# Kernel optimization log

Hardware: AMD Instinct MI355X
Metric: run time of the kernel (lower is better)

The kernel has to match this reference:

```python
import jax, jax.numpy as jnp
import numpy as np

HIDDEN_DIM = 1024
NUM_HEADS = 16
HEAD_DIM = HIDDEN_DIM // NUM_HEADS


def setup_inputs() -> dict:
    key = jax.random.key(0)
    k1, k2, k3 = jax.random.split(key, 3)
    B, S, D = 2, 2048, HIDDEN_DIM
    x = jax.random.normal(k1, (B, S, D), dtype=jnp.float32)
    attention_mask = jnp.ones((B, S), dtype=jnp.int32)
    scale = 1.0 / np.sqrt(D)
    W_qkv = jax.random.normal(k2, (D, 3 * D), dtype=jnp.float32) * scale
    b_qkv = jnp.zeros((3 * D,), dtype=jnp.float32)
    W_out = jax.random.normal(k3, (D, D), dtype=jnp.float32) * scale
    b_out = jnp.zeros((D,), dtype=jnp.float32)
    return {"x": x, "attention_mask": attention_mask,
            "W_qkv": W_qkv, "b_qkv": b_qkv, "W_out": W_out, "b_out": b_out}


def reference(x, attention_mask, W_qkv, b_qkv, W_out, b_out):
    B, S, D = x.shape
    H, hd = NUM_HEADS, HEAD_DIM
    qkv = x @ W_qkv + b_qkv                     # [B,S,3D]
    # Faithful to torch: view to [B,S,H,3*hd] THEN chunk last dim (per-head interleaving)
    qkv = qkv.reshape(B, S, H, 3 * hd)
    q, k, v = jnp.split(qkv, 3, axis=-1)        # each [B,S,H,hd]
    scores = jnp.einsum('bqhd,bkhd->bhqk', q, k) / np.sqrt(hd)  # [B,H,S,S]
    mask = attention_mask[:, None, None, :]     # broadcast over heads, queries
    scores = jnp.where(mask == 0, -jnp.inf, scores)
    weights = jax.nn.softmax(scores, axis=-1)
    out = jnp.einsum('bhqk,bkhd->bqhd', weights, v).reshape(B, S, D)
    return out @ W_out + b_out
```

## Files before the change

kernel.cpp:

```cpp
#include <hip/hip_runtime.h>

#define SDIM 2048
#define NHEADS 16
#define HD 64

typedef __attribute__((ext_vector_type(8))) short bf16x8;
typedef __attribute__((ext_vector_type(8))) unsigned short u16x8;
typedef __attribute__((ext_vector_type(4))) float f32x4;
typedef unsigned short u16;

static __device__ __forceinline__ u16 f2bf(float f) {
  unsigned u = __builtin_bit_cast(unsigned, f);
  u += 0x7fffu + ((u >> 16) & 1u);
  return (u16)(u >> 16);
}

static __device__ __forceinline__ unsigned cvt_pk_bf16(float lo, float hi) {
  unsigned r;
  asm("v_cvt_pk_bf16_f32 %0, %1, %2" : "=v"(r) : "v"(lo), "v"(hi));
  return r;
}

static __device__ __forceinline__ f32x4 mfma16(bf16x8 a, bf16x8 b, f32x4 c) {
  return __builtin_amdgcn_mfma_f32_16x16x32_bf16(a, b, c, 0, 0, 0);
}

static __device__ __forceinline__ void gload16(const u16* g, u16* l) {
  __builtin_amdgcn_global_load_lds(
      (const __attribute__((address_space(1))) void*)g,
      (__attribute__((address_space(3))) void*)l, 16, 0, 0);
}

__global__ void cvt_kernel(const float* __restrict__ in, u16* __restrict__ out, int n8) {
  int i = blockIdx.x * blockDim.x + threadIdx.x;
  if (i >= n8) return;
  const float4* p = (const float4*)(in + (long)i * 8);
  float4 a = p[0], b = p[1];
  u16x8 r;
  r[0] = f2bf(a.x); r[1] = f2bf(a.y); r[2] = f2bf(a.z); r[3] = f2bf(a.w);
  r[4] = f2bf(b.x); r[5] = f2bf(b.y); r[6] = f2bf(b.z); r[7] = f2bf(b.w);
  *(u16x8*)(out + (long)i * 8) = r;
}

__global__ void transpose_cvt(const float* __restrict__ W, u16* __restrict__ Wt, int K, int N) {
  __shared__ float t[32][33];
  int tx = threadIdx.x & 31, ty = threadIdx.x >> 5;
  int n0 = blockIdx.x * 32, k0 = blockIdx.y * 32;
#pragma unroll
  for (int i = 0; i < 32; i += 8) t[ty + i][tx] = W[(long)(k0 + ty + i) * N + n0 + tx];
  __syncthreads();
#pragma unroll
  for (int i = 0; i < 32; i += 8) Wt[(long)(n0 + ty + i) * K + k0 + tx] = f2bf(t[tx][ty + i]);
}

__global__ __launch_bounds__(256) void vtrans_kernel(const u16* __restrict__ QKV,
                                                     u16* __restrict__ Vt) {
  __shared__ u16 t[64][72];
  const int bh = blockIdx.y, s0 = blockIdx.x * 64;
  const int b = bh >> 4, h = bh & 15;
  const u16* src = QKV + ((long)(b * SDIM + s0)) * 3072 + h * 192 + 128;
  int r = threadIdx.x >> 3, c = (threadIdx.x & 7) * 8;
  *(uint4*)&t[r][c]      = *(const uint4*)(src + (long)r * 3072 + c);
  *(uint4*)&t[r + 32][c] = *(const uint4*)(src + (long)(r + 32) * 3072 + c);
  __syncthreads();
  int d = threadIdx.x >> 2, sc = (threadIdx.x & 3) * 16;
  u16 tmp[16];
#pragma unroll
  for (int k = 0; k < 16; ++k) tmp[k] = t[sc + k][d];
  u16* dst = Vt + ((long)(bh * HD + d)) * SDIM + s0 + sc;
  *(uint4*)dst = *(uint4*)&tmp[0];
  *(uint4*)(dst + 8) = *(uint4*)&tmp[8];
}

template <int EPI>
__global__ __launch_bounds__(256) void gemm_bf16(
    const u16* __restrict__ A, const u16* __restrict__ Bt,
    const float* __restrict__ bias, float* __restrict__ Cf, u16* __restrict__ Cb,
    int M, int N, int K)
{
  __shared__ __align__(16) u16 As[128 * 64];
  __shared__ __align__(16) u16 Bs[128 * 64];
  const int tid = threadIdx.x, lane = tid & 63, wid = tid >> 6;
  const int wm = wid >> 1, wn = wid & 1;
  const int l15 = lane & 15, l4 = lane >> 4;
  const int nblk = gridDim.x;
  const int lb = (blockIdx.x & 7) * (nblk >> 3) + (blockIdx.x >> 3);
  const int nx = N >> 7;
  const int m0 = (lb / nx) * 128, n0 = (lb % nx) * 128;
  const int srow = lane >> 3;
  const int schunk = (lane & 7) ^ srow;

  f32x4 acc[4][4];
#pragma unroll
  for (int i = 0; i < 4; ++i)
#pragma unroll
    for (int j = 0; j < 4; ++j) acc[i][j] = {0.f, 0.f, 0.f, 0.f};

  const int nk = K >> 6;
  for (int kt = 0; kt < nk; ++kt) {
    const int kc = kt << 6;
#pragma unroll
    for (int is = 0; is < 4; ++is) {
      int rb = wid * 32 + is * 8;
      int r = rb + srow;
      gload16(A  + (long)(m0 + r) * K + kc + schunk * 8, &As[rb * 64]);
      gload16(Bt + (long)(n0 + r) * K + kc + schunk * 8, &Bs[rb * 64]);
    }
    asm volatile("s_waitcnt vmcnt(0)" ::: "memory");
    __syncthreads();
#pragma unroll
    for (int kk = 0; kk < 2; ++kk) {
      bf16x8 af[4], bfr[4];
#pragma unroll
      for (int mt = 0; mt < 4; ++mt) {
        int row = wm * 64 + mt * 16 + l15;
        af[mt] = *(const bf16x8*)&As[row * 64 + (((kk * 4 + l4) ^ (l15 & 7)) * 8)];
      }
#pragma unroll
      for (int nt = 0; nt < 4; ++nt) {
        int row = wn * 64 + nt * 16 + l15;
        bfr[nt] = *(const bf16x8*)&Bs[row * 64 + (((kk * 4 + l4) ^ (l15 & 7)) * 8)];
      }
#pragma unroll
      for (int mt = 0; mt < 4; ++mt)
#pragma unroll
        for (int nt = 0; nt < 4; ++nt)
          acc[mt][nt] = mfma16(af[mt], bfr[nt], acc[mt][nt]);
    }
    __syncthreads();
  }

#pragma unroll
  for (int mt = 0; mt < 4; ++mt)
#pragma unroll
    for (int nt = 0; nt < 4; ++nt)
#pragma unroll
      for (int r = 0; r < 4; ++r) {
        int row = m0 + wm * 64 + mt * 16 + l4 * 4 + r;
        int col = n0 + wn * 64 + nt * 16 + l15;
        float v = acc[mt][nt][r] + bias[col];
        if (EPI == 0) Cf[(long)row * N + col] = v;
        else          Cb[(long)row * N + col] = f2bf(v);
      }
}

__global__ __launch_bounds__(256) void attn_kernel(
    const u16* __restrict__ QKV, const u16* __restrict__ Vtg,
    const int* __restrict__ maskg, u16* __restrict__ Og)
{
  __shared__ __align__(16) u16 Ks[2][64][64];
  __shared__ __align__(16) u16 Vs[2][64][64];
  __shared__ __align__(16) u16 Ps[64][64];
  const int tid = threadIdx.x, lane = tid & 63, w = tid >> 6;
  const int l15 = lane & 15, l4 = lane >> 4;
  const int lb = (blockIdx.x & 7) * 128 + (blockIdx.x >> 3);
  const int qt = lb & 31, bh = lb >> 5;
  const int b = bh >> 4, h = bh & 15;
  const u16* Qp = QKV + ((long)(b * SDIM + qt * 64)) * 3072 + h * 192;
  const u16* Kp = QKV + (long)(b * SDIM) * 3072 + h * 192 + 64;
  const u16* Vp = Vtg + (long)bh * HD * SDIM;
  const float SC = 0.18033688011112042f;
  const int NT = SDIM / 64;

  bf16x8 qa[2];
#pragma unroll
  for (int ks = 0; ks < 2; ++ks)
    qa[ks] = *(const bf16x8*)(Qp + (long)(w * 16 + l15) * 3072 + ks * 32 + l4 * 8);

  f32x4 O[4];
  float lsum[4];
#pragma unroll
  for (int dt = 0; dt < 4; ++dt) O[dt] = {0.f, 0.f, 0.f, 0.f};
#pragma unroll
  for (int r = 0; r < 4; ++r) lsum[r] = 0.f;

  char* KsB = (char*)&Ks[0][0][0];
  char* VsB = (char*)&Vs[0][0][0];
  char* PsB = (char*)&Ps[0][0];
  const int srow = lane >> 3;
  const int schunk = (lane & 7) ^ srow;

  u16* kDst[2][2] = { { (u16*)(KsB + w * 2048),        (u16*)(KsB + w * 2048 + 1024) },
                      { (u16*)(KsB + 8192 + w * 2048), (u16*)(KsB + 8192 + w * 2048 + 1024) } };
  u16* vDst[2][2] = { { (u16*)(VsB + w * 2048),        (u16*)(VsB + w * 2048 + 1024) },
                      { (u16*)(VsB + 8192 + w * 2048), (u16*)(VsB + 8192 + w * 2048 + 1024) } };
  const u16* kS0 = Kp + (long)(w * 16 + srow) * 3072 + schunk * 8;
  const u16* kS1 = Kp + (long)(w * 16 + 8 + srow) * 3072 + schunk * 8;
  const u16* vS0 = Vp + (long)(w * 16 + srow) * SDIM + schunk * 8;
  const u16* vS1 = Vp + (long)(w * 16 + 8 + srow) * SDIM + schunk * 8;
  const int* mrow = maskg + b * SDIM + l15;

  int off[2][4];
#pragma unroll
  for (int j = 0; j < 2; ++j)
#pragma unroll
    for (int x = 0; x < 4; ++x)
      off[j][x] = (x * 16 + l15) * 128 + (((j * 4 + l4) ^ (l15 & 7)) << 4);
  int poffr[2];
#pragma unroll
  for (int j = 0; j < 2; ++j)
    poffr[j] = (w * 16 + l15) * 128 + (((j * 4 + l4) ^ (l15 & 7)) << 4);
  int pw[4][4];
#pragma unroll
  for (int r = 0; r < 4; ++r) {
    int prow = w * 16 + l4 * 4 + r, rx = prow & 7, ch = l15 >> 3;
    int rbase = prow * 128 + (l15 & 7) * 2;
#pragma unroll
    for (int c = 0; c < 4; ++c) pw[r][c] = rbase + (((2 * c + ch) ^ rx) << 4);
  }

  gload16(kS0, kDst[0][0]); gload16(kS1, kDst[0][1]);
  gload16(vS0, vDst[0][0]); gload16(vS1, vDst[0][1]);
  kS0 += 64 * 3072; kS1 += 64 * 3072; vS0 += 64; vS1 += 64;
  asm volatile("s_waitcnt vmcnt(0)" ::: "memory");
  __syncthreads();

  for (int kt = 0; kt < NT; ++kt) {
    const int cur = kt & 1;
    if (kt + 1 < NT) {
      gload16(kS0, kDst[cur ^ 1][0]); gload16(kS1, kDst[cur ^ 1][1]);
      gload16(vS0, vDst[cur ^ 1][0]); gload16(vS1, vDst[cur ^ 1][1]);
      kS0 += 64 * 3072; kS1 += 64 * 3072; vS0 += 64; vS1 += 64;
    }

    float mbM[4];
#pragma unroll
    for (int nt = 0; nt < 4; ++nt)
      mbM[nt] = (mrow[nt * 16] ? 0.f : -1e30f) - 12.0f;
    mrow += 64;

    const char* Kc = KsB + cur * 8192;
    const char* Vc = VsB + cur * 8192;

    f32x4 sc4[4];
    __builtin_amdgcn_s_setprio(1);
#pragma unroll
    for (int nt = 0; nt < 4; ++nt) {
      bf16x8 kb0 = *(const bf16x8*)(Kc + off[0][nt]);
      bf16x8 kb1 = *(const bf16x8*)(Kc + off[1][nt]);
      f32x4 z = {0.f, 0.f, 0.f, 0.f};
      z = mfma16(qa[0], kb0, z);
      z = mfma16(qa[1], kb1, z);
      sc4[nt] = z;
    }
    __builtin_amdgcn_s_setprio(0);

#pragma unroll
    for (int r = 0; r < 4; ++r) {
      float p0 = __builtin_amdgcn_exp2f(sc4[0][r] * SC + mbM[0]);
      float p1 = __builtin_amdgcn_exp2f(sc4[1][r] * SC + mbM[1]);
      float p2 = __builtin_amdgcn_exp2f(sc4[2][r] * SC + mbM[2]);
      float p3 = __builtin_amdgcn_exp2f(sc4[3][r] * SC + mbM[3]);
      lsum[r] += (p0 + p1) + (p2 + p3);
      unsigned u01 = cvt_pk_bf16(p0, p1);
      unsigned u23 = cvt_pk_bf16(p2, p3);
      *(u16*)(PsB + pw[r][0]) = (u16)u01;
      *(u16*)(PsB + pw[r][1]) = (u16)(u01 >> 16);
      *(u16*)(PsB + pw[r][2]) = (u16)u23;
      *(u16*)(PsB + pw[r][3]) = (u16)(u23 >> 16);
    }
    asm volatile("s_waitcnt lgkmcnt(0)" ::: "memory");
    __builtin_amdgcn_sched_barrier(0);

    __builtin_amdgcn_s_setprio(1);
#pragma unroll
    for (int ks2 = 0; ks2 < 2; ++ks2) {
      bf16x8 pa = *(const bf16x8*)(PsB + poffr[ks2]);
#pragma unroll
      for (int dt = 0; dt < 4; ++dt) {
        bf16x8 vb = *(const bf16x8*)(Vc + off[ks2][dt]);
        O[dt] = mfma16(pa, vb, O[dt]);
      }
    }
    __builtin_amdgcn_s_setprio(0);
    __syncthreads();
  }

  float inv[4];
#pragma unroll
  for (int r = 0; r < 4; ++r) {
    float s = lsum[r];
#pragma unroll
    for (int off2 = 1; off2 < 16; off2 <<= 1) s += __shfl_xor(s, off2);
    inv[r] = 1.0f / s;
  }

#pragma unroll
  for (int dt = 0; dt < 4; ++dt)
#pragma unroll
    for (int r = 0; r < 4; ++r) {
      int s = qt * 64 + w * 16 + l4 * 4 + r;
      int d = dt * 16 + l15;
      Og[((long)(b * SDIM + s)) * 1024 + h * HD + d] = f2bf(O[dt][r] * inv[r]);
    }
}

extern "C" void kernel_launch(void* const* d_in, const int* in_sizes, int n_in,
                              void* d_out, int out_size, void* d_ws, size_t ws_size,
                              hipStream_t stream) {
  const float* x    = (const float*)d_in[0];
  const int*   am   = (const int*)d_in[1];
  const float* Wqkv = (const float*)d_in[2];
  const float* bqkv = (const float*)d_in[3];
  const float* Wout = (const float*)d_in[4];
  const float* bout = (const float*)d_in[5];
  float* out = (float*)d_out;
  char* ws = (char*)d_ws;

  u16* xb   = (u16*)(ws);
  u16* AOb  = (u16*)(ws);
  u16* wqt  = (u16*)(ws + (size_t) 8 * 1024 * 1024);
  u16* wot  = (u16*)(ws + (size_t)14 * 1024 * 1024);
  u16* QKVb = (u16*)(ws + (size_t)16 * 1024 * 1024);
  u16* Vtb  = (u16*)(ws + (size_t)40 * 1024 * 1024);

  cvt_kernel<<<2048, 256, 0, stream>>>(x, xb, 524288);
  transpose_cvt<<<dim3(96, 32), 256, 0, stream>>>(Wqkv, wqt, 1024, 3072);
  transpose_cvt<<<dim3(32, 32), 256, 0, stream>>>(Wout, wot, 1024, 1024);
  gemm_bf16<1><<<768, 256, 0, stream>>>(xb, wqt, bqkv, nullptr, QKVb,
                                        4096, 3072, 1024);
  vtrans_kernel<<<dim3(32, 32), 256, 0, stream>>>(QKVb, Vtb);
  attn_kernel<<<1024, 256, 0, stream>>>(QKVb, Vtb, am, AOb);
  gemm_bf16<0><<<256, 256, 0, stream>>>(AOb, wot, bout, out, nullptr,
                                        4096, 1024, 1024);
}
```

Before: 151.9 us.

## Process 128 query rows per attention block to reuse K/V tiles

Each attention workgroup now handles 128 query rows instead of 64, with every wave computing two 16-row tiles. Each K/V tile loaded into shared memory then feeds twice as many MFMAs, which halves global K/V traffic and barrier count per unit of work. In exchange the grid halves to 512 blocks, so fewer blocks are available to fill the CUs, and register use and shared memory for P grow.

```diff
diff --git a/kernel.cpp b/kernel.cpp
--- a/kernel.cpp
+++ b/kernel.cpp
@@ -150,29 +150,34 @@
 {
   __shared__ __align__(16) u16 Ks[2][64][64];
   __shared__ __align__(16) u16 Vs[2][64][64];
-  __shared__ __align__(16) u16 Ps[64][64];
+  __shared__ __align__(16) u16 Ps[128][64];
   const int tid = threadIdx.x, lane = tid & 63, w = tid >> 6;
   const int l15 = lane & 15, l4 = lane >> 4;
-  const int lb = (blockIdx.x & 7) * 128 + (blockIdx.x >> 3);
-  const int qt = lb & 31, bh = lb >> 5;
+  const int lb = (blockIdx.x & 7) * 64 + (blockIdx.x >> 3);
+  const int qt = lb & 15, bh = lb >> 4;
   const int b = bh >> 4, h = bh & 15;
-  const u16* Qp = QKV + ((long)(b * SDIM + qt * 64)) * 3072 + h * 192;
+  const u16* Qp = QKV + ((long)(b * SDIM + qt * 128)) * 3072 + h * 192;
   const u16* Kp = QKV + (long)(b * SDIM) * 3072 + h * 192 + 64;
   const u16* Vp = Vtg + (long)bh * HD * SDIM;
   const float SC = 0.18033688011112042f;
   const int NT = SDIM / 64;
 
-  bf16x8 qa[2];
-#pragma unroll
-  for (int ks = 0; ks < 2; ++ks)
-    qa[ks] = *(const bf16x8*)(Qp + (long)(w * 16 + l15) * 3072 + ks * 32 + l4 * 8);
-
-  f32x4 O[4];
-  float lsum[4];
-#pragma unroll
-  for (int dt = 0; dt < 4; ++dt) O[dt] = {0.f, 0.f, 0.f, 0.f};
-#pragma unroll
-  for (int r = 0; r < 4; ++r) lsum[r] = 0.f;
+  bf16x8 qa[2][2];
+#pragma unroll
+  for (int rt = 0; rt < 2; ++rt)
+#pragma unroll
+    for (int ks = 0; ks < 2; ++ks)
+      qa[rt][ks] = *(const bf16x8*)(Qp + (long)(w * 32 + rt * 16 + l15) * 3072 + ks * 32 + l4 * 8);
+
+  f32x4 O[2][4];
+  float lsum[2][4];
+#pragma unroll
+  for (int rt = 0; rt < 2; ++rt) {
+#pragma unroll
+    for (int dt = 0; dt < 4; ++dt) O[rt][dt] = {0.f, 0.f, 0.f, 0.f};
+#pragma unroll
+    for (int r = 0; r < 4; ++r) lsum[rt][r] = 0.f;
+  }
 
   char* KsB = (char*)&Ks[0][0][0];
   char* VsB = (char*)&Vs[0][0][0];
@@ -180,10 +185,6 @@
   const int srow = lane >> 3;
   const int schunk = (lane & 7) ^ srow;
 
-  u16* kDst[2][2] = { { (u16*)(KsB + w * 2048),        (u16*)(KsB + w * 2048 + 1024) },
-                      { (u16*)(KsB + 8192 + w * 2048), (u16*)(KsB + 8192 + w * 2048 + 1024) } };
-  u16* vDst[2][2] = { { (u16*)(VsB + w * 2048),        (u16*)(VsB + w * 2048 + 1024) },
-                      { (u16*)(VsB + 8192 + w * 2048), (u16*)(VsB + 8192 + w * 2048 + 1024) } };
   const u16* kS0 = Kp + (long)(w * 16 + srow) * 3072 + schunk * 8;
   const u16* kS1 = Kp + (long)(w * 16 + 8 + srow) * 3072 + schunk * 8;
   const u16* vS0 = Vp + (long)(w * 16 + srow) * SDIM + schunk * 8;
@@ -196,21 +197,29 @@
 #pragma unroll
     for (int x = 0; x < 4; ++x)
       off[j][x] = (x * 16 + l15) * 128 + (((j * 4 + l4) ^ (l15 & 7)) << 4);
-  int poffr[2];
-#pragma unroll
-  for (int j = 0; j < 2; ++j)
-    poffr[j] = (w * 16 + l15) * 128 + (((j * 4 + l4) ^ (l15 & 7)) << 4);
-  int pw[4][4];
-#pragma unroll
-  for (int r = 0; r < 4; ++r) {
-    int prow = w * 16 + l4 * 4 + r, rx = prow & 7, ch = l15 >> 3;
-    int rbase = prow * 128 + (l15 & 7) * 2;
-#pragma unroll
-    for (int c = 0; c < 4; ++c) pw[r][c] = rbase + (((2 * c + ch) ^ rx) << 4);
+  int poffr[2][2];
+#pragma unroll
+  for (int rt = 0; rt < 2; ++rt)
+#pragma unroll
+    for (int j = 0; j < 2; ++j)
+      poffr[rt][j] = (w * 32 + rt * 16 + l15) * 128 + (((j * 4 + l4) ^ (l15 & 7)) << 4);
+  int pw[2][4][4];
+#pragma unroll
+  for (int rt = 0; rt < 2; ++rt)
+#pragma unroll
+    for (int r = 0; r < 4; ++r) {
+      int prow = w * 32 + rt * 16 + l4 * 4 + r, rx = prow & 7, ch = l15 >> 3;
+      int rbase = prow * 128 + (l15 & 7) * 2;
+#pragma unroll
+      for (int c = 0; c < 4; ++c) pw[rt][r][c] = rbase + (((2 * c + ch) ^ rx) << 4);
+    }
+
+  {
+    u16* kd = (u16*)(KsB + w * 2048);
+    u16* vd = (u16*)(VsB + w * 2048);
+    gload16(kS0, kd); gload16(kS1, kd + 512);
+    gload16(vS0, vd); gload16(vS1, vd + 512);
   }
-
-  gload16(kS0, kDst[0][0]); gload16(kS1, kDst[0][1]);
-  gload16(vS0, vDst[0][0]); gload16(vS1, vDst[0][1]);
   kS0 += 64 * 3072; kS1 += 64 * 3072; vS0 += 64; vS1 += 64;
   asm volatile("s_waitcnt vmcnt(0)" ::: "memory");
   __syncthreads();
@@ -218,8 +227,10 @@
   for (int kt = 0; kt < NT; ++kt) {
     const int cur = kt & 1;
     if (kt + 1 < NT) {
-      gload16(kS0, kDst[cur ^ 1][0]); gload16(kS1, kDst[cur ^ 1][1]);
-      gload16(vS0, vDst[cur ^ 1][0]); gload16(vS1, vDst[cur ^ 1][1]);
+      u16* kd = (u16*)(KsB + (cur ^ 1) * 8192 + w * 2048);
+      u16* vd = (u16*)(VsB + (cur ^ 1) * 8192 + w * 2048);
+      gload16(kS0, kd); gload16(kS1, kd + 512);
+      gload16(vS0, vd); gload16(vS1, vd + 512);
       kS0 += 64 * 3072; kS1 += 64 * 3072; vS0 += 64; vS1 += 64;
     }
 
@@ -232,67 +243,78 @@
     const char* Kc = KsB + cur * 8192;
     const char* Vc = VsB + cur * 8192;
 
-    f32x4 sc4[4];
+    f32x4 sc4[2][4];
     __builtin_amdgcn_s_setprio(1);
 #pragma unroll
     for (int nt = 0; nt < 4; ++nt) {
       bf16x8 kb0 = *(const bf16x8*)(Kc + off[0][nt]);
       bf16x8 kb1 = *(const bf16x8*)(Kc + off[1][nt]);
-      f32x4 z = {0.f, 0.f, 0.f, 0.f};
-      z = mfma16(qa[0], kb0, z);
-      z = mfma16(qa[1], kb1, z);
-      sc4[nt] = z;
+#pragma unroll
+      for (int rt = 0; rt < 2; ++rt) {
+        f32x4 z = {0.f, 0.f, 0.f, 0.f};
+        z = mfma16(qa[rt][0], kb0, z);
+        z = mfma16(qa[rt][1], kb1, z);
+        sc4[rt][nt] = z;
+      }
     }
     __builtin_amdgcn_s_setprio(0);
 
 #pragma unroll
-    for (int r = 0; r < 4; ++r) {
-      float p0 = __builtin_amdgcn_exp2f(sc4[0][r] * SC + mbM[0]);
-      float p1 = __builtin_amdgcn_exp2f(sc4[1][r] * SC + mbM[1]);
-      float p2 = __builtin_amdgcn_exp2f(sc4[2][r] * SC + mbM[2]);
-      float p3 = __builtin_amdgcn_exp2f(sc4[3][r] * SC + mbM[3]);
-      lsum[r] += (p0 + p1) + (p2 + p3);
-      unsigned u01 = cvt_pk_bf16(p0, p1);
-      unsigned u23 = cvt_pk_bf16(p2, p3);
-      *(u16*)(PsB + pw[r][0]) = (u16)u01;
-      *(u16*)(PsB + pw[r][1]) = (u16)(u01 >> 16);
-      *(u16*)(PsB + pw[r][2]) = (u16)u23;
-      *(u16*)(PsB + pw[r][3]) = (u16)(u23 >> 16);
-    }
+    for (int rt = 0; rt < 2; ++rt)
+#pragma unroll
+      for (int r = 0; r < 4; ++r) {
+        float p0 = __builtin_amdgcn_exp2f(sc4[rt][0][r] * SC + mbM[0]);
+        float p1 = __builtin_amdgcn_exp2f(sc4[rt][1][r] * SC + mbM[1]);
+        float p2 = __builtin_amdgcn_exp2f(sc4[rt][2][r] * SC + mbM[2]);
+        float p3 = __builtin_amdgcn_exp2f(sc4[rt][3][r] * SC + mbM[3]);
+        lsum[rt][r] += (p0 + p1) + (p2 + p3);
+        unsigned u01 = cvt_pk_bf16(p0, p1);
+        unsigned u23 = cvt_pk_bf16(p2, p3);
+        *(u16*)(PsB + pw[rt][r][0]) = (u16)u01;
+        *(u16*)(PsB + pw[rt][r][1]) = (u16)(u01 >> 16);
+        *(u16*)(PsB + pw[rt][r][2]) = (u16)u23;
+        *(u16*)(PsB + pw[rt][r][3]) = (u16)(u23 >> 16);
+      }
     asm volatile("s_waitcnt lgkmcnt(0)" ::: "memory");
     __builtin_amdgcn_sched_barrier(0);
 
     __builtin_amdgcn_s_setprio(1);
 #pragma unroll
     for (int ks2 = 0; ks2 < 2; ++ks2) {
-      bf16x8 pa = *(const bf16x8*)(PsB + poffr[ks2]);
+      bf16x8 pa0 = *(const bf16x8*)(PsB + poffr[0][ks2]);
+      bf16x8 pa1 = *(const bf16x8*)(PsB + poffr[1][ks2]);
 #pragma unroll
       for (int dt = 0; dt < 4; ++dt) {
         bf16x8 vb = *(const bf16x8*)(Vc + off[ks2][dt]);
-        O[dt] = mfma16(pa, vb, O[dt]);
+        O[0][dt] = mfma16(pa0, vb, O[0][dt]);
+        O[1][dt] = mfma16(pa1, vb, O[1][dt]);
       }
     }
     __builtin_amdgcn_s_setprio(0);
     __syncthreads();
   }
 
-  float inv[4];
-#pragma unroll
-  for (int r = 0; r < 4; ++r) {
-    float s = lsum[r];
-#pragma unroll
-    for (int off2 = 1; off2 < 16; off2 <<= 1) s += __shfl_xor(s, off2);
-    inv[r] = 1.0f / s;
-  }
-
-#pragma unroll
-  for (int dt = 0; dt < 4; ++dt)
+  float inv[2][4];
+#pragma unroll
+  for (int rt = 0; rt < 2; ++rt)
 #pragma unroll
     for (int r = 0; r < 4; ++r) {
-      int s = qt * 64 + w * 16 + l4 * 4 + r;
-      int d = dt * 16 + l15;
-      Og[((long)(b * SDIM + s)) * 1024 + h * HD + d] = f2bf(O[dt][r] * inv[r]);
-    }
+      float s = lsum[rt][r];
+#pragma unroll
+      for (int off2 = 1; off2 < 16; off2 <<= 1) s += __shfl_xor(s, off2);
+      inv[rt][r] = 1.0f / s;
+    }
+
+#pragma unroll
+  for (int rt = 0; rt < 2; ++rt)
+#pragma unroll
+    for (int dt = 0; dt < 4; ++dt)
+#pragma unroll
+      for (int r = 0; r < 4; ++r) {
+        int s = qt * 128 + w * 32 + rt * 16 + l4 * 4 + r;
+        int d = dt * 16 + l15;
+        Og[((long)(b * SDIM + s)) * 1024 + h * HD + d] = f2bf(O[rt][dt][r] * inv[rt][r]);
+      }
 }
 
 extern "C" void kernel_launch(void* const* d_in, const int* in_sizes, int n_in,
@@ -320,7 +342,7 @@
   gemm_bf16<1><<<768, 256, 0, stream>>>(xb, wqt, bqkv, nullptr, QKVb,
                                         4096, 3072, 1024);
   vtrans_kernel<<<dim3(32, 32), 256, 0, stream>>>(QKVb, Vtb);
-  attn_kernel<<<1024, 256, 0, stream>>>(QKVb, Vtb, am, AOb);
+  attn_kernel<<<512, 256, 0, stream>>>(QKVb, Vtb, am, AOb);
   gemm_bf16<0><<<256, 256, 0, stream>>>(AOb, wot, bout, out, nullptr,
                                         4096, 1024, 1024);
 }
```

Result: no change. 149.7 us (-1.4%).
